# Kernel tuning notes

Measured on AMD Instinct MI355X. Metric: run time of the kernel, lower is better.

Reference implementation:

```python
import jax, jax.numpy as jnp
import numpy as np

EPS = 1e-12
NUM_IDS = 25          # instance ids 0..24 (0 = background)
INTER_MARGIN = 0.2
W_SEM_ALIGN, W_SEM_MEM, W_INS_CON, W_INS_MEM = 0.5, 1.0, 1.0, 1.0


def _l2norm(x, axis):
    return x / jnp.maximum(jnp.linalg.norm(x, axis=axis, keepdims=True), EPS)


def _flat_pix(x):  # [B,T,C,H,W] -> [B*T*H*W, C]
    B, T, C, H, W = x.shape
    return jnp.transpose(x, (0, 1, 3, 4, 2)).reshape(B * T * H * W, C)


def _seg_ids(mask_r):  # [B,T,Hp,Wp] int -> [BT*N] global segment ids
    B, T, Hp, Wp = mask_r.shape
    bt = jnp.arange(B * T, dtype=jnp.int32)[:, None] * NUM_IDS
    return (mask_r.reshape(B * T, Hp * Wp) + bt).reshape(-1)


def _mask_nearest_half(inst_mask):
    # torch nearest interp H -> H/2 picks src index floor(i*2) = 2i
    return inst_mask[:, :, ::2, ::2]


def _gt_bilinear_half(x):
    B, T, C, H, W = x.shape
    return x.reshape(B, T, C, H // 2, 2, W // 2, 2).mean(axis=(4, 6))


def _sem_align_loss(refined_sem, lseg_gt, inst_mask):
    # fused replacement of the per-(b,t,instance) python loops: one segment-reduce pass
    B, T, C, Hp, Wp = refined_sem.shape
    mask_r = _mask_nearest_half(inst_mask)
    gt = _l2norm(_gt_bilinear_half(lseg_gt), axis=2)
    pred = _l2norm(refined_sem, axis=2)
    predf, gtf = _flat_pix(pred), _flat_pix(gt)
    seg = _seg_ids(mask_r)
    nseg = B * T * NUM_IDS
    sums = jax.ops.segment_sum(gtf, seg, num_segments=nseg)
    cnts = jax.ops.segment_sum(jnp.ones_like(seg, jnp.float32), seg, num_segments=nseg)
    # normalize(mean) == normalize(sum); prototype is detached in the original
    proto = jax.lax.stop_gradient(_l2norm(sums, axis=1))
    cos_loss = 1.0 - jnp.sum(predf * proto[seg], axis=1)
    valid = (mask_r.reshape(-1) > 0) & (cnts[seg] >= 2.0)
    total = jnp.sum(jnp.where(valid, cos_loss, 0.0))
    count = jnp.maximum(jnp.sum(valid.astype(jnp.float32)), 1.0)
    return total / count


def _memory_loss(pred_feat, mem_feat, mem_mask):
    pred = _l2norm(pred_feat, axis=2)
    tgt = jax.lax.stop_gradient(_l2norm(mem_feat, axis=2))
    cos_dist = (1.0 - jnp.sum(pred * tgt, axis=2, keepdims=True)) * mem_mask
    return jnp.sum(cos_dist) / jnp.maximum(jnp.sum(mem_mask), 1.0)


def _ins_contrastive_loss(refined_ins, inst_mask):
    # ContrastiveLoss(inter_mode='hinge', inter_margin=0.2, normalize_feats=True)
    B, T, C, Hp, Wp = refined_ins.shape
    mask_r = _mask_nearest_half(inst_mask)
    feat = _l2norm(refined_ins, axis=2)
    featf = _flat_pix(feat)
    seg = _seg_ids(mask_r)
    nseg = B * T * NUM_IDS
    sums = jax.ops.segment_sum(featf, seg, num_segments=nseg)
    cnts = jax.ops.segment_sum(jnp.ones_like(seg, jnp.float32), seg, num_segments=nseg)
    proto = _l2norm(sums, axis=1)  # [BT*K, C]
    # intra: pull pixels toward their instance prototype
    cos_loss = 1.0 - jnp.sum(featf * proto[seg], axis=1)
    valid = (mask_r.reshape(-1) > 0) & (cnts[seg] >= 2.0)
    intra = jnp.sum(jnp.where(valid, cos_loss, 0.0)) / jnp.maximum(
        jnp.sum(valid.astype(jnp.float32)), 1.0)
    # inter: hinge pushing apart prototypes of different instances within a scene
    P = proto.reshape(B * T, NUM_IDS, C)
    vmask = (cnts.reshape(B * T, NUM_IDS) >= 2.0) & (jnp.arange(NUM_IDS)[None, :] > 0)
    sim = jnp.einsum('bkc,blc->bkl', P, P)
    pair = vmask[:, :, None] & vmask[:, None, :] & ~jnp.eye(NUM_IDS, dtype=bool)[None]
    hinge = jnp.maximum(sim - INTER_MARGIN, 0.0)
    inter = jnp.sum(jnp.where(pair, hinge, 0.0)) / jnp.maximum(
        jnp.sum(pair.astype(jnp.float32)), 1.0)
    return intra + inter


def setup_inputs() -> dict:
    key = jax.random.key(0)
    ks = jax.random.split(key, 7)
    B, T, C_SEM, C_INS, HP, WP = 2, 4, 512, 64, 64, 64
    H, W = 2 * HP, 2 * WP
    return {
        "refined_sem": jax.random.normal(ks[0], (B, T, C_SEM, HP, WP), jnp.float32),
        "refined_ins": jax.random.normal(ks[1], (B, T, C_INS, HP, WP), jnp.float32),
        "lseg_gt": jax.random.normal(ks[2], (B, T, C_SEM, H, W), jnp.float32),
        "mem_sem": jax.random.normal(ks[3], (B, T, C_SEM, HP, WP), jnp.float32),
        "mem_ins": jax.random.normal(ks[4], (B, T, C_INS, HP, WP), jnp.float32),
        "mem_mask": (jax.random.uniform(ks[5], (B, T, 1, HP, WP)) < 0.7).astype(jnp.float32),
        "inst_mask": jax.random.randint(ks[6], (B, T, H, W), 0, NUM_IDS, dtype=jnp.int32),
    }


def reference(refined_sem, refined_ins, lseg_gt, mem_sem, mem_ins, mem_mask, inst_mask):
    sem_align = _sem_align_loss(refined_sem, lseg_gt, inst_mask)
    sem_mem = _memory_loss(refined_sem, mem_sem, mem_mask)
    ins_con = _ins_contrastive_loss(refined_ins, inst_mask)
    ins_mem = _memory_loss(refined_ins, mem_ins, mem_mask)
    objective = (W_SEM_ALIGN * sem_align + W_SEM_MEM * sem_mem
                 + W_INS_CON * ins_con + W_INS_MEM * ins_mem)
    return objective
```

## Files before the change

kernel.cpp:

```cpp
#include <hip/hip_runtime.h>

typedef unsigned short u16;
typedef unsigned int u32;
typedef unsigned long long u64;

#define NID 25


#define SC16  65536.0f
#define ISC16 (1.0f/65536.0f)
#define SC20  1048576.0f
#define ISC20 (1.0f/1048576.0f)
#define SC32  4294967296.0f

__device__ __forceinline__ float bf2f(u16 h){ return __uint_as_float(((u32)h) << 16); }
__device__ __forceinline__ u16 f2bf(float f){
  u32 u = __float_as_uint(f);
  u32 r = u + 0x7fffu + ((u >> 16) & 1u);
  return (u16)(r >> 16);
}

template<bool BF>
__device__ __forceinline__ float LD(const void* p, size_t i){
  if constexpr (BF) return bf2f(((const u16*)p)[i]);
  else return ((const float*)p)[i];
}
template<bool BF>
__device__ __forceinline__ float2 LD2(const void* p, size_t i){
  if constexpr (BF){
    ushort2 v = *(const ushort2*)((const u16*)p + i);
    return make_float2(bf2f(v.x), bf2f(v.y));
  } else {
    return *(const float2*)((const float*)p + i);
  }
}
template<bool BF>
__device__ __forceinline__ float4 LD4(const void* p, size_t i){
  if constexpr (BF){
    ushort4 v = *(const ushort4*)((const u16*)p + i);
    return make_float4(bf2f(v.x), bf2f(v.y), bf2f(v.z), bf2f(v.w));
  } else {
    return *(const float4*)((const float*)p + i);
  }
}

__global__ __launch_bounds__(256) void k_probe(const u32* __restrict__ x,
                                               int* __restrict__ flag){
  __shared__ int cnt;
  if (threadIdx.x == 0) cnt = 0;
  __syncthreads();
  int c = 0;
  for (int i = threadIdx.x; i < 1024; i += 256){
    u32 e = (x[i] >> 7) & 0xffu;
    c += (e >= 100 && e <= 140) ? 1 : 0;
  }
  atomicAdd(&cnt, c);
  __syncthreads();
  if (threadIdx.x == 0) *flag = (cnt >= 600) ? 1 : 0;
}

template<bool BF>
__device__ void p1a_body(const void* lg, int* __restrict__ ss){
  __shared__ int ps[64];
  const int t = threadIdx.x;
  const int hr = blockIdx.x;
  const int cg = blockIdx.y;
  const int bt = blockIdx.z;
  const int q2 = t & 31;
  const int cw = t >> 5;
  if (t < 64) ps[t] = 0;
  __syncthreads();
  float s0 = 0.f, s1 = 0.f;
  const int c0 = cg*64 + cw*8;
  #pragma unroll
  for (int k = 0; k < 8; ++k){
    const size_t o = ((size_t)(bt*512 + c0 + k) << 14) + (hr << 8) + (q2 << 2);
    float4 a = LD4<BF>(lg, o);
    float4 b = LD4<BF>(lg, o + 128);
    const float m0 = (a.x + a.y + b.x + b.y) * 0.25f;
    const float m1 = (a.z + a.w + b.z + b.w) * 0.25f;
    s0 += m0*m0; s1 += m1*m1;
  }
  atomicAdd(&ps[q2*2],     (int)rintf(s0 * SC20));
  atomicAdd(&ps[q2*2 + 1], (int)rintf(s1 * SC20));
  __syncthreads();
  if (t < 64){
    const int v = ps[t];
    if (v) atomicAdd(&ss[(bt << 12) + (hr << 6) + t], v);
  }
}

template<bool BF>
__device__ void p4_body(const void* ri, const int* __restrict__ im,
                        int* __restrict__ ins_sums, int qb){
  __shared__ int   sums[2*25*33];
  __shared__ float parts[2][128];
  const int t = threadIdx.x;
  const int pb = qb * 128;
  const int bt = pb >> 12;
  const int h = t >> 7, q = t & 127;
  const int p = (pb + q) & 4095;
  const int id = im[(bt << 14) + ((p >> 6) << 8) + ((p & 63) << 1)];
  for (int k = t; k < 2*25*33; k += 256) sums[k] = 0;
  float vals[32];
  float ffh = 0.f;
  #pragma unroll
  for (int cc = 0; cc < 32; ++cc){
    float v = LD<BF>(ri, (size_t)(bt*64 + h*32 + cc)*4096 + p);
    vals[cc] = v; ffh += v*v;
  }
  parts[h][q] = ffh;
  __syncthreads();
  const float inv = SC16 / fmaxf(sqrtf(parts[0][q] + parts[1][q]), 1e-12f);
  int* dst = &sums[h*825 + id*33];
  #pragma unroll
  for (int cc = 0; cc < 32; ++cc) atomicAdd(&dst[cc], (int)rintf(vals[cc]*inv));
  __syncthreads();
  for (int k = t; k < 1600; k += 256){
    const int id2 = k >> 6, c2 = k & 63, h2 = c2 >> 5, cc2 = c2 & 31;
    const int v = sums[h2*825 + id2*33 + cc2];
    if (v) atomicAdd(&ins_sums[(bt*NID + id2)*64 + c2], v);
  }
}

template<bool BF>
__device__ void a_body(const void* lg, int* ss, const void* ri,
                       const int* im, int* ins_sums){
  if (blockIdx.z < 8){
    p1a_body<BF>(lg, ss);
  } else {
    const int q = blockIdx.y*64 + blockIdx.x;
    if (q < 256) p4_body<BF>(ri, im, ins_sums, q);
  }
}
__global__ __launch_bounds__(256) void k_a(const void* lg, int* ss,
    const void* ri, const int* im, int* ins_sums, const int* flag){
  if (*flag) a_body<true>(lg, ss, ri, im, ins_sums);
  else       a_body<false>(lg, ss, ri, im, ins_sums);
}

template<bool BF>
__device__ void p1b_body(const void* lg, const int* __restrict__ im,
                         const int* __restrict__ ss,
                         int* __restrict__ sem_sums, int* __restrict__ cnts){
  __shared__ int sums[4*25*129];
  __shared__ float invl[128];
  __shared__ int hist[NID];
  const int t = threadIdx.x;
  const int bt = blockIdx.y;
  const int pxb = blockIdx.x * 128;
  const int q = t & 127;
  const int cw = t >> 7;
  for (int k = t; k < 4*25*129; k += 512) sums[k] = 0;
  if (t < NID) hist[t] = 0;
  const int p = pxb + q;
  const int id = im[(bt << 14) + ((p >> 6) << 8) + ((p & 63) << 1)];
  if (t < 128){
    const float sf = (float)ss[(bt << 12) + pxb + t] * ISC20;
    invl[t] = SC16 / fmaxf(sqrtf(sf), 1e-12f);
  }
  __syncthreads();
  if (t < 128) atomicAdd(&hist[id], 1);
  const float inv = invl[q];
  const size_t pbase = ((size_t)(bt*512 + cw*128) << 14)
                     + ((p >> 6) << 8) + ((p & 63) << 1);
  int* dst = &sums[(cw*25 + id)*129];
  #pragma unroll 8
  for (int k = 0; k < 128; ++k){
    const size_t o = pbase + ((size_t)k << 14);
    float2 a = LD2<BF>(lg, o);
    float2 b = LD2<BF>(lg, o + 128);
    const float m = (a.x + a.y + b.x + b.y) * 0.25f;
    atomicAdd(&dst[k], (int)rintf(m * inv));
  }
  __syncthreads();
  for (int k = t; k < 25*512; k += 512){
    const int id2 = k >> 9, c2 = k & 511, cw2 = c2 >> 7, k2 = c2 & 127;
    const int v = sums[(cw2*25 + id2)*129 + k2];
    if (v) atomicAdd(&sem_sums[(bt*NID + id2)*512 + c2], v);
  }
  if (t < NID && hist[t] > 0) atomicAdd(&cnts[bt*NID + t], hist[t]);
}
__global__ __launch_bounds__(512) void k_p1b(const void* lg, const int* im,
    const int* ss, int* sem_sums, int* cnts, const int* flag){
  if (*flag) p1b_body<true>(lg, im, ss, sem_sums, cnts);
  else       p1b_body<false>(lg, im, ss, sem_sums, cnts);
}

__global__ __launch_bounds__(256) void k_p5(const int* __restrict__ sem_sums,
    const int* __restrict__ ins_sums, const int* __restrict__ cnts,
    float* __restrict__ proto_sem, float* __restrict__ proto_ins,
    int* __restrict__ valid_tab){
  const int wg = blockIdx.x*4 + (threadIdx.x >> 6);
  const int l  = threadIdx.x & 63;
  if (blockIdx.x < 50){
    const int seg = wg;
    float v[8]; float ss = 0.f;
    const size_t base = (size_t)seg*512 + l;
    #pragma unroll
    for (int k = 0; k < 8; ++k){
      v[k] = (float)sem_sums[base + 64*k] * ISC16;
      ss += v[k]*v[k];
    }
    for (int m = 1; m < 64; m <<= 1) ss += __shfl_xor(ss, m, 64);
    const float inv = 1.f / fmaxf(sqrtf(ss), 1e-12f);
    #pragma unroll
    for (int k = 0; k < 8; ++k) proto_sem[base + 64*k] = v[k]*inv;
    if (l == 0) valid_tab[seg] = (cnts[seg] >= 2 && (seg % NID) != 0) ? 1 : 0;
  } else {
    const int seg = wg - 200;
    float v = (float)ins_sums[(size_t)seg*64 + l] * ISC16;
    float ss = v*v;
    for (int m = 1; m < 64; m <<= 1) ss += __shfl_xor(ss, m, 64);
    proto_ins[(size_t)seg*64 + l] = v * (1.f / fmaxf(sqrtf(ss), 1e-12f));
  }
}

template<bool BF>
__device__ void p3n_body(const void* rs, const void* ms, const void* mmask,
    const int* __restrict__ im, const float* __restrict__ proto_sem,
    const int* __restrict__ valid_tab, u64* __restrict__ sc, float4* parts){
  const int t = threadIdx.x;
  const int pb = blockIdx.x * 32;
  const int bt = pb >> 12;
  const int px0 = pb & 4095;
  const int w  = t >> 4;
  const int l2 = t & 15;
  const int p0 = px0 + 2*l2, p1 = p0 + 1;
  const int id0 = im[(bt << 14) + ((p0 >> 6) << 8) + ((p0 & 63) << 1)];
  const int id1 = im[(bt << 14) + ((p1 >> 6) << 8) + ((p1 & 63) << 1)];
  const float* __restrict__ pr0 = proto_sem + ((size_t)(bt*NID + id0) << 9) + w*32;
  const float* __restrict__ pr1 = proto_sem + ((size_t)(bt*NID + id1) << 9) + w*32;
  const size_t cbase = ((size_t)(bt*512 + w*32) << 12) + p0;
  float pp0=0.f,pp1=0.f,pm0=0.f,pm1=0.f,mm0=0.f,mm1=0.f,pd0=0.f,pd1=0.f;
  #pragma unroll 8
  for (int cc = 0; cc < 32; ++cc){
    float2 pv = LD2<BF>(rs, cbase + ((size_t)cc << 12));
    float2 mv = LD2<BF>(ms, cbase + ((size_t)cc << 12));
    pp0 += pv.x*pv.x; pp1 += pv.y*pv.y;
    mm0 += mv.x*mv.x; mm1 += mv.y*mv.y;
    pm0 += pv.x*mv.x; pm1 += pv.y*mv.y;
    pd0 += pv.x*pr0[cc]; pd1 += pv.y*pr1[cc];
  }
  #pragma unroll
  for (int m = 16; m <= 32; m <<= 1){
    pp0 += __shfl_xor(pp0, m, 64); pp1 += __shfl_xor(pp1, m, 64);
    pm0 += __shfl_xor(pm0, m, 64); pm1 += __shfl_xor(pm1, m, 64);
    mm0 += __shfl_xor(mm0, m, 64); mm1 += __shfl_xor(mm1, m, 64);
    pd0 += __shfl_xor(pd0, m, 64); pd1 += __shfl_xor(pd1, m, 64);
  }
  const int lane = t & 63, wv = t >> 6;
  if (lane < 16){
    parts[wv*32 + 2*lane]     = make_float4(pp0, pm0, mm0, pd0);
    parts[wv*32 + 2*lane + 1] = make_float4(pp1, pm1, mm1, pd1);
  }
  __syncthreads();
  if (t < 32){
    float4 s0 = parts[t], s1 = parts[32+t], s2 = parts[64+t], s3 = parts[96+t];
    const float ppn = s0.x+s1.x+s2.x+s3.x;
    const float pm  = s0.y+s1.y+s2.y+s3.y;
    const float mm  = s0.z+s1.z+s2.z+s3.z;
    const float pd  = s0.w+s1.w+s2.w+s3.w;
    const int p = px0 + t, g = pb + t;
    const int id = im[(bt << 14) + ((p >> 6) << 8) + ((p & 63) << 1)];
    const int vld = valid_tab[bt*NID + id];
    const float npn = fmaxf(sqrtf(ppn), 1e-12f);
    float a_i = vld ? (1.f - pd/npn) : 0.f;
    float vc  = vld ? 1.f : 0.f;
    float mkv = LD<BF>(mmask, g);
    const float nmn = fmaxf(sqrtf(mm), 1e-12f);
    float s_i = mkv * (1.f - pm/(npn*nmn));
    #pragma unroll
    for (int m = 1; m < 32; m <<= 1){
      a_i += __shfl_xor(a_i, m, 32);
      vc  += __shfl_xor(vc,  m, 32);
      s_i += __shfl_xor(s_i, m, 32);
      mkv += __shfl_xor(mkv, m, 32);
    }
    if (t == 0){
      long long v0 = llrintf(a_i * SC32);
      long long v2 = llrintf(s_i * SC32);
      if (v0) atomicAdd(&sc[0], (u64)v0);
      if (vc != 0.f) atomicAdd(&sc[1], (u64)llrintf(vc));
      if (v2) atomicAdd(&sc[2], (u64)v2);
      if (mkv != 0.f) atomicAdd(&sc[3], (u64)llrintf(mkv));
    }
  }
}

template<bool BF>
__device__ void p6n_body(const void* ri, const void* mi, const void* mmask,
    const int* __restrict__ im, const float* __restrict__ proto_ins,
    const int* __restrict__ valid_tab, u64* __restrict__ sc, float4* parts){
  const int t = threadIdx.x;
  const int bx = (int)blockIdx.x - 1024;
  const int pb = bx * 64;
  const int bt = pb >> 12;
  const int px0 = pb & 4095;
  const int h  = t >> 5;
  const int l2 = t & 31;
  const int p0 = px0 + 2*l2, p1 = p0 + 1;
  const int id0 = im[(bt << 14) + ((p0 >> 6) << 8) + ((p0 & 63) << 1)];
  const int id1 = im[(bt << 14) + ((p1 >> 6) << 8) + ((p1 & 63) << 1)];
  const float* __restrict__ pr0 = proto_ins + (size_t)(bt*NID + id0)*64 + h*8;
  const float* __restrict__ pr1 = proto_ins + (size_t)(bt*NID + id1)*64 + h*8;
  const size_t cbase = ((size_t)(bt*64 + h*8) << 12) + p0;
  float ff0=0.f,ff1=0.f,fm0=0.f,fm1=0.f,m20=0.f,m21=0.f,fd0=0.f,fd1=0.f;
  #pragma unroll
  for (int cc = 0; cc < 8; ++cc){
    float2 fv = LD2<BF>(ri, cbase + ((size_t)cc << 12));
    float2 mv = LD2<BF>(mi, cbase + ((size_t)cc << 12));
    ff0 += fv.x*fv.x; ff1 += fv.y*fv.y;
    m20 += mv.x*mv.x; m21 += mv.y*mv.y;
    fm0 += fv.x*mv.x; fm1 += fv.y*mv.y;
    fd0 += fv.x*pr0[cc]; fd1 += fv.y*pr1[cc];
  }
  ff0 += __shfl_xor(ff0, 32, 64); ff1 += __shfl_xor(ff1, 32, 64);
  fm0 += __shfl_xor(fm0, 32, 64); fm1 += __shfl_xor(fm1, 32, 64);
  m20 += __shfl_xor(m20, 32, 64); m21 += __shfl_xor(m21, 32, 64);
  fd0 += __shfl_xor(fd0, 32, 64); fd1 += __shfl_xor(fd1, 32, 64);
  const int lane = t & 63, wv = t >> 6;
  if (lane < 32){
    parts[wv*64 + 2*lane]     = make_float4(ff0, fm0, m20, fd0);
    parts[wv*64 + 2*lane + 1] = make_float4(ff1, fm1, m21, fd1);
  }
  __syncthreads();
  if (t < 64){
    float4 s0 = parts[t], s1 = parts[64+t], s2 = parts[128+t], s3 = parts[192+t];
    const float ff = s0.x+s1.x+s2.x+s3.x;
    const float fm = s0.y+s1.y+s2.y+s3.y;
    const float m2 = s0.z+s1.z+s2.z+s3.z;
    const float fd = s0.w+s1.w+s2.w+s3.w;
    const int p = px0 + t, g = pb + t;
    const int id = im[(bt << 14) + ((p >> 6) << 8) + ((p & 63) << 1)];
    const int vld = valid_tab[bt*NID + id];
    const float nf = fmaxf(sqrtf(ff), 1e-12f);
    float ii = vld ? (1.f - fd/nf) : 0.f;
    float mkv = LD<BF>(mmask, g);
    const float nm = fmaxf(sqrtf(m2), 1e-12f);
    float mi_ = mkv * (1.f - fm/(nf*nm));
    #pragma unroll
    for (int m = 1; m < 64; m <<= 1){
      ii  += __shfl_xor(ii,  m, 64);
      mi_ += __shfl_xor(mi_, m, 64);
    }
    if (t == 0){
      long long v4 = llrintf(ii  * SC32);
      long long v5 = llrintf(mi_ * SC32);
      if (v4) atomicAdd(&sc[4], (u64)v4);
      if (v5) atomicAdd(&sc[5], (u64)v5);
    }
  }
}

__device__ void fh_body(const float* __restrict__ proto_ins,
                        const int* __restrict__ valid_tab, u64* __restrict__ sc,
                        float* P, int* vt, float* red){
  const int bt = (int)blockIdx.x - 1536;
  const int t = threadIdx.x;
  for (int f = t; f < 1600; f += 256){
    P[(f >> 6)*65 + (f & 63)] = proto_ins[bt*1600 + f];
  }
  if (t < NID) vt[t] = valid_tab[bt*NID + t];
  __syncthreads();
  float hsum = 0.f, pcnt = 0.f;
  for (int kl = t; kl < 625; kl += 256){
    const int k = kl / 25, l = kl - k*25;
    if (k != l && vt[k] && vt[l]){
      float s = 0.f;
      #pragma unroll
      for (int c = 0; c < 64; ++c) s += P[k*65 + c] * P[l*65 + c];
      hsum += fmaxf(s - 0.2f, 0.f);
      pcnt += 1.f;
    }
  }
  for (int m = 1; m < 64; m <<= 1){
    hsum += __shfl_xor(hsum, m, 64);
    pcnt += __shfl_xor(pcnt, m, 64);
  }
  if ((t & 63) == 0){ red[t >> 6] = hsum; red[4 + (t >> 6)] = pcnt; }
  __syncthreads();
  if (t == 0){
    const float h  = red[0]+red[1]+red[2]+red[3];
    const float pc = red[4]+red[5]+red[6]+red[7];
    long long v6 = llrintf(h * SC32);
    if (v6) atomicAdd(&sc[6], (u64)v6);
    if (pc != 0.f) atomicAdd(&sc[7], (u64)llrintf(pc));
  }
}

template<bool BF>
__device__ void tail_body(const void* rs, const void* ms, const void* ri,
    const void* mi, const void* mmask, const int* im,
    const float* proto_sem, const float* proto_ins, const int* valid_tab,
    u64* sc, float4* parts3, float4* parts6, float* P, int* vt, float* red){
  const u32 bx = blockIdx.x;
  if (bx < 1024)      p3n_body<BF>(rs, ms, mmask, im, proto_sem, valid_tab, sc, parts3);
  else if (bx < 1536) p6n_body<BF>(ri, mi, mmask, im, proto_ins, valid_tab, sc, parts6);
  else                fh_body(proto_ins, valid_tab, sc, P, vt, red);
}
__global__ __launch_bounds__(256) void k_tail(const void* rs, const void* ms,
    const void* ri, const void* mi, const void* mmask, const int* im,
    const float* proto_sem, const float* proto_ins, const int* valid_tab,
    u64* sc, const int* flag){
  __shared__ float4 parts3[128];
  __shared__ float4 parts6[256];
  __shared__ float  P[25*65];
  __shared__ int    vt[NID];
  __shared__ float  red[8];
  if (*flag) tail_body<true>(rs, ms, ri, mi, mmask, im, proto_sem, proto_ins,
                             valid_tab, sc, parts3, parts6, P, vt, red);
  else       tail_body<false>(rs, ms, ri, mi, mmask, im, proto_sem, proto_ins,
                              valid_tab, sc, parts3, parts6, P, vt, red);
}

__global__ __launch_bounds__(64) void k_f2(const u64* __restrict__ sc,
                                           u32* __restrict__ out){
  if (threadIdx.x == 0){
    const double S = 1.0 / 4294967296.0;
    const double asum = (double)(long long)sc[0] * S;
    const double vcnt = (double)(long long)sc[1];
    const double ssum = (double)(long long)sc[2] * S;
    const double mcnt = (double)(long long)sc[3];
    const double isum = (double)(long long)sc[4] * S;
    const double msum = (double)(long long)sc[5] * S;
    const double hsum = (double)(long long)sc[6] * S;
    const double pc   = (double)(long long)sc[7];
    const double align = asum / (vcnt > 1.0 ? vcnt : 1.0);
    const double smem  = ssum / (mcnt > 1.0 ? mcnt : 1.0);
    const double intra = isum / (vcnt > 1.0 ? vcnt : 1.0);
    const double imem  = msum / (mcnt > 1.0 ? mcnt : 1.0);
    const double interv = hsum / (pc > 1.0 ? pc : 1.0);
    const double obj = 0.5*align + smem + intra + interv + imem;
    const u32 b = (u32)f2bf((float)obj);
    out[0] = (b << 16) | b;
  }
}

extern "C" void kernel_launch(void* const* d_in, const int* in_sizes, int n_in,
                              void* d_out, int out_size, void* d_ws, size_t ws_size,
                              hipStream_t stream){
  const void* rs    = d_in[0];
  const void* ri    = d_in[1];
  const void* lg    = d_in[2];
  const void* ms    = d_in[3];
  const void* mi    = d_in[4];
  const void* mmask = d_in[5];
  const int*  im    = (const int*)d_in[6];

  char* ws = (char*)d_ws;
  u64*   sc        = (u64*)  ws;
  int*   flag      = (int*)  (ws + 64);
  int*   cnts      = (int*)  (ws + 256);
  int*   sem_sums  = (int*)  (ws + 4096);
  int*   ins_sums  = (int*)  (ws + 413696);
  int*   ssq       = (int*)  (ws + 466944);
  float* proto_sem = (float*)(ws + 466944);
  float* proto_ins = (float*)(ws + 876544);
  int*   valid_tab = (int*)  (ws + 927744);

  hipMemsetAsync(d_ws, 0, 598016, stream);
  k_probe<<<1, 256, 0, stream>>>((const u32*)rs, flag);
  k_a<<<dim3(64, 8, 9), 256, 0, stream>>>(lg, ssq, ri, im, ins_sums, flag);
  k_p1b<<<dim3(32, 8), 512, 0, stream>>>(lg, im, ssq, sem_sums, cnts, flag);
  k_p5<<<100, 256, 0, stream>>>(sem_sums, ins_sums, cnts, proto_sem, proto_ins, valid_tab);
  k_tail<<<1544, 256, 0, stream>>>(rs, ms, ri, mi, mmask, im, proto_sem,
                                   proto_ins, valid_tab, sc, flag);
  k_f2<<<1, 64, 0, stream>>>(sc, (u32*)d_out);
}
```

Baseline: 581.8 us.

## Fuse lseg norm and segment-sum passes into one read of lseg_gt

Merges the separate squared-norm pass and the segment accumulation pass over lseg_gt into a single kernel. Each block keeps the downsampled means for one half-resolution row in registers as packed bf16, reduces the per-pixel norm in shared memory, then does the segment atomics. This removes a second full read of the largest input. It splits the instance-sum work into its own launch, and storing the means in bf16 adds rounding error.

```diff
diff --git a/kernel.cpp b/kernel.cpp
--- a/kernel.cpp
+++ b/kernel.cpp
@@ -9,8 +9,6 @@
 
 #define SC16  65536.0f
 #define ISC16 (1.0f/65536.0f)
-#define SC20  1048576.0f
-#define ISC20 (1.0f/1048576.0f)
 #define SC32  4294967296.0f
 
 __device__ __forceinline__ float bf2f(u16 h){ return __uint_as_float(((u32)h) << 16); }
@@ -34,15 +32,6 @@
     return *(const float2*)((const float*)p + i);
   }
 }
-template<bool BF>
-__device__ __forceinline__ float4 LD4(const void* p, size_t i){
-  if constexpr (BF){
-    ushort4 v = *(const ushort4*)((const u16*)p + i);
-    return make_float4(bf2f(v.x), bf2f(v.y), bf2f(v.z), bf2f(v.w));
-  } else {
-    return *(const float4*)((const float*)p + i);
-  }
-}
 
 __global__ __launch_bounds__(256) void k_probe(const u32* __restrict__ x,
                                                int* __restrict__ flag){
@@ -60,43 +49,82 @@
 }
 
 template<bool BF>
-__device__ void p1a_body(const void* lg, int* __restrict__ ss){
-  __shared__ int ps[64];
-  const int t = threadIdx.x;
+__device__ void p1_body(const void* lg, const int* __restrict__ im,
+                        int* __restrict__ sem_sums, int* __restrict__ cnts){
+  __shared__ int   sums[8*25*65];
+  __shared__ float pp[8*64];
+  __shared__ float invl[64];
+  __shared__ int   hist[NID];
+  const int t = threadIdx.x, g = t >> 6, q = t & 63;
+  const int bt = blockIdx.y;
   const int hr = blockIdx.x;
-  const int cg = blockIdx.y;
-  const int bt = blockIdx.z;
-  const int q2 = t & 31;
-  const int cw = t >> 5;
-  if (t < 64) ps[t] = 0;
-  __syncthreads();
-  float s0 = 0.f, s1 = 0.f;
-  const int c0 = cg*64 + cw*8;
+
+  for (int k = t; k < 8*25*65; k += 512) sums[k] = 0;
+  if (t < NID) hist[t] = 0;
+  __syncthreads();
+
+  u32 mr[32];
+  float ps = 0.f;
+  const size_t base = ((size_t)(bt*512 + g*64) << 14) + (hr << 8) + (q << 1);
   #pragma unroll
-  for (int k = 0; k < 8; ++k){
-    const size_t o = ((size_t)(bt*512 + c0 + k) << 14) + (hr << 8) + (q2 << 2);
-    float4 a = LD4<BF>(lg, o);
-    float4 b = LD4<BF>(lg, o + 128);
-    const float m0 = (a.x + a.y + b.x + b.y) * 0.25f;
-    const float m1 = (a.z + a.w + b.z + b.w) * 0.25f;
-    s0 += m0*m0; s1 += m1*m1;
-  }
-  atomicAdd(&ps[q2*2],     (int)rintf(s0 * SC20));
-  atomicAdd(&ps[q2*2 + 1], (int)rintf(s1 * SC20));
+  for (int c8 = 0; c8 < 8; ++c8){
+    float2 a[8], b[8];
+    #pragma unroll
+    for (int k = 0; k < 8; ++k){
+      const size_t o = base + ((size_t)(c8*8 + k) << 14);
+      a[k] = LD2<BF>(lg, o);
+      b[k] = LD2<BF>(lg, o + 128);
+    }
+    #pragma unroll
+    for (int k = 0; k < 8; ++k){
+      const float m = (a[k].x + a[k].y + b[k].x + b[k].y) * 0.25f;
+      ps += m*m;
+      const int cc = c8*8 + k;
+      u16 mb = f2bf(m);
+      if (cc & 1) mr[cc>>1] |= ((u32)mb << 16);
+      else        mr[cc>>1]  = (u32)mb;
+    }
+  }
+  pp[g*64 + q] = ps;
   __syncthreads();
   if (t < 64){
-    const int v = ps[t];
-    if (v) atomicAdd(&ss[(bt << 12) + (hr << 6) + t], v);
-  }
+    float s = 0.f;
+    #pragma unroll
+    for (int k = 0; k < 8; ++k) s += pp[k*64 + t];
+    invl[t] = SC16 / fmaxf(sqrtf(s), 1e-12f);
+  }
+  __syncthreads();
+  const int id = im[(bt << 14) + (hr << 8) + (q << 1)];
+  if (g == 0) atomicAdd(&hist[id], 1);
+  const float inv = invl[q];
+  int* dst = &sums[g*1625 + id*65];
+  #pragma unroll 8
+  for (int cc = 0; cc < 64; ++cc){
+    u16 mb = (cc & 1) ? (u16)(mr[cc>>1] >> 16) : (u16)(mr[cc>>1] & 0xffffu);
+    atomicAdd(&dst[cc], (int)rintf(bf2f(mb) * inv));
+  }
+  __syncthreads();
+
+  for (int k = t; k < 25*512; k += 512){
+    const int id2 = k >> 9, c2 = k & 511, g2 = c2 >> 6, cc2 = c2 & 63;
+    const int v = sums[g2*1625 + id2*65 + cc2];
+    if (v) atomicAdd(&sem_sums[(bt*NID + id2)*512 + c2], v);
+  }
+  if (t < NID && hist[t] > 0) atomicAdd(&cnts[bt*NID + t], hist[t]);
+}
+__global__ __launch_bounds__(512, 4) void k_p1(const void* lg, const int* im,
+    int* sem_sums, int* cnts, const int* flag){
+  if (*flag) p1_body<true>(lg, im, sem_sums, cnts);
+  else       p1_body<false>(lg, im, sem_sums, cnts);
 }
 
 template<bool BF>
 __device__ void p4_body(const void* ri, const int* __restrict__ im,
-                        int* __restrict__ ins_sums, int qb){
+                        int* __restrict__ ins_sums){
   __shared__ int   sums[2*25*33];
   __shared__ float parts[2][128];
   const int t = threadIdx.x;
-  const int pb = qb * 128;
+  const int pb = blockIdx.x * 128;
   const int bt = pb >> 12;
   const int h = t >> 7, q = t & 127;
   const int p = (pb + q) & 4095;
@@ -122,69 +150,10 @@
     if (v) atomicAdd(&ins_sums[(bt*NID + id2)*64 + c2], v);
   }
 }
-
-template<bool BF>
-__device__ void a_body(const void* lg, int* ss, const void* ri,
-                       const int* im, int* ins_sums){
-  if (blockIdx.z < 8){
-    p1a_body<BF>(lg, ss);
-  } else {
-    const int q = blockIdx.y*64 + blockIdx.x;
-    if (q < 256) p4_body<BF>(ri, im, ins_sums, q);
-  }
-}
-__global__ __launch_bounds__(256) void k_a(const void* lg, int* ss,
-    const void* ri, const int* im, int* ins_sums, const int* flag){
-  if (*flag) a_body<true>(lg, ss, ri, im, ins_sums);
-  else       a_body<false>(lg, ss, ri, im, ins_sums);
-}
-
-template<bool BF>
-__device__ void p1b_body(const void* lg, const int* __restrict__ im,
-                         const int* __restrict__ ss,
-                         int* __restrict__ sem_sums, int* __restrict__ cnts){
-  __shared__ int sums[4*25*129];
-  __shared__ float invl[128];
-  __shared__ int hist[NID];
-  const int t = threadIdx.x;
-  const int bt = blockIdx.y;
-  const int pxb = blockIdx.x * 128;
-  const int q = t & 127;
-  const int cw = t >> 7;
-  for (int k = t; k < 4*25*129; k += 512) sums[k] = 0;
-  if (t < NID) hist[t] = 0;
-  const int p = pxb + q;
-  const int id = im[(bt << 14) + ((p >> 6) << 8) + ((p & 63) << 1)];
-  if (t < 128){
-    const float sf = (float)ss[(bt << 12) + pxb + t] * ISC20;
-    invl[t] = SC16 / fmaxf(sqrtf(sf), 1e-12f);
-  }
-  __syncthreads();
-  if (t < 128) atomicAdd(&hist[id], 1);
-  const float inv = invl[q];
-  const size_t pbase = ((size_t)(bt*512 + cw*128) << 14)
-                     + ((p >> 6) << 8) + ((p & 63) << 1);
-  int* dst = &sums[(cw*25 + id)*129];
-  #pragma unroll 8
-  for (int k = 0; k < 128; ++k){
-    const size_t o = pbase + ((size_t)k << 14);
-    float2 a = LD2<BF>(lg, o);
-    float2 b = LD2<BF>(lg, o + 128);
-    const float m = (a.x + a.y + b.x + b.y) * 0.25f;
-    atomicAdd(&dst[k], (int)rintf(m * inv));
-  }
-  __syncthreads();
-  for (int k = t; k < 25*512; k += 512){
-    const int id2 = k >> 9, c2 = k & 511, cw2 = c2 >> 7, k2 = c2 & 127;
-    const int v = sums[(cw2*25 + id2)*129 + k2];
-    if (v) atomicAdd(&sem_sums[(bt*NID + id2)*512 + c2], v);
-  }
-  if (t < NID && hist[t] > 0) atomicAdd(&cnts[bt*NID + t], hist[t]);
-}
-__global__ __launch_bounds__(512) void k_p1b(const void* lg, const int* im,
-    const int* ss, int* sem_sums, int* cnts, const int* flag){
-  if (*flag) p1b_body<true>(lg, im, ss, sem_sums, cnts);
-  else       p1b_body<false>(lg, im, ss, sem_sums, cnts);
+__global__ __launch_bounds__(256) void k_p4(const void* ri, const int* im,
+    int* ins_sums, const int* flag){
+  if (*flag) p4_body<true>(ri, im, ins_sums);
+  else       p4_body<false>(ri, im, ins_sums);
 }
 
 __global__ __launch_bounds__(256) void k_p5(const int* __restrict__ sem_sums,
@@ -454,15 +423,14 @@
   int*   cnts      = (int*)  (ws + 256);
   int*   sem_sums  = (int*)  (ws + 4096);
   int*   ins_sums  = (int*)  (ws + 413696);
-  int*   ssq       = (int*)  (ws + 466944);
   float* proto_sem = (float*)(ws + 466944);
   float* proto_ins = (float*)(ws + 876544);
   int*   valid_tab = (int*)  (ws + 927744);
 
-  hipMemsetAsync(d_ws, 0, 598016, stream);
+  hipMemsetAsync(d_ws, 0, 464896, stream);
   k_probe<<<1, 256, 0, stream>>>((const u32*)rs, flag);
-  k_a<<<dim3(64, 8, 9), 256, 0, stream>>>(lg, ssq, ri, im, ins_sums, flag);
-  k_p1b<<<dim3(32, 8), 512, 0, stream>>>(lg, im, ssq, sem_sums, cnts, flag);
+  k_p1<<<dim3(64, 8), 512, 0, stream>>>(lg, im, sem_sums, cnts, flag);
+  k_p4<<<256, 256, 0, stream>>>(ri, im, ins_sums, flag);
   k_p5<<<100, 256, 0, stream>>>(sem_sums, ins_sums, cnts, proto_sem, proto_ins, valid_tab);
   k_tail<<<1544, 256, 0, stream>>>(rs, ms, ri, mi, mmask, im, proto_sem,
                                    proto_ins, valid_tab, sc, flag);
```

New measurement: 527.2 us. 9.4% less time.
